# Optimization experiments

Hardware: AMD Instinct MI355X
Metric: run time of the kernel (lower is better)

## Reference

```python
import jax, jax.numpy as jnp
import numpy as np

DELTA = 0.1


def setup_inputs() -> dict:
    key = jax.random.key(0)
    k1, k2 = jax.random.split(key)
    B, T_text, adim, T_feats = 16, 512, 256, 4096
    hs = jax.random.normal(k1, (B, T_text, adim), dtype=jnp.float32)
    ds = jax.random.uniform(k2, (B, T_text), dtype=jnp.float32) * 8.0  # durations in frames
    h_masks = jnp.ones((B, T_feats), dtype=bool)
    d_masks = jnp.ones((B, T_text), dtype=bool)
    return {"hs": hs, "ds": ds, "h_masks": h_masks, "d_masks": d_masks}


def reference(hs, ds, h_masks, d_masks):
    # hs: (B, T_text, adim), ds: (B, T_text), h_masks: (B, T_feats), d_masks: (B, T_text)
    B, T_feats = h_masks.shape
    t = jnp.arange(T_feats, dtype=jnp.float32)[None, :] * h_masks.astype(jnp.float32)  # (B, T_feats)
    c = jnp.cumsum(ds, axis=-1) - ds / 2  # token centers (B, T_text)
    # energy: (B, T_feats, T_text) -- the large broadcast intermediate
    energy = -DELTA * (t[:, :, None] - c[:, None, :]) ** 2
    energy = jnp.where(d_masks[:, None, :], energy, -jnp.inf)
    p_attn = jax.nn.softmax(energy, axis=2)  # (B, T_feats, T_text)
    return jnp.einsum('bft,bta->bfa', p_attn, hs)  # (B, T_feats, adim)
```

## Files before the change

### kernel.cpp

```cpp
#include <hip/hip_runtime.h>


namespace {
constexpr int kB = 16;
constexpr int kT = 512;
constexpr int kA = 256;
constexpr int kF = 4096;
constexpr float kDelta = 0.1f;
constexpr int kFTile = 16;
constexpr int kRadius = 10;
constexpr int kPad = 4;
constexpr int kMaxK = 128;
constexpr int kWStride = kFTile + 4;
typedef float f32x4 __attribute__((ext_vector_type(4)));
}

__global__ __launch_bounds__(256, 7) void upsample_kernel(
    const float* __restrict__ hs, const float* __restrict__ ds,
    const int* __restrict__ h_masks, const int* __restrict__ d_masks,
    float* __restrict__ out) {
  __shared__ __align__(16) float s_c[kT];
  __shared__ int s_dm[kT];
  __shared__ __align__(16) float s_w[kMaxK * kWStride];
  __shared__ float s_t[kFTile];
  __shared__ float s_rsum[kFTile];
  __shared__ float s_wsum[4];

  const int id = blockIdx.x;
  const int b = id & 15;
  const int f0 = (id >> 4) * kFTile;
  const int tid = threadIdx.x;
  const int wave = tid >> 6, lane = tid & 63;

  const float2 dsv = *reinterpret_cast<const float2*>(ds + (size_t)b * kT + 2 * tid);
  const float psum = dsv.x + dsv.y;
  float incl = psum;
#pragma unroll
  for (int off = 1; off < 64; off <<= 1) {
    float u = __shfl_up(incl, off, 64);
    if (lane >= off) incl += u;
  }
  if (lane == 63) s_wsum[wave] = incl;

  for (int j = tid; j < kT; j += 256) s_dm[j] = d_masks[(size_t)b * kT + j];

  const int g = tid >> 4;
  const int l = tid & 15;
  const int f = f0 + g;
  const float tf = h_masks[(size_t)b * kF + f] ? (float)f : 0.0f;
  __syncthreads();

  float basesum = 0.0f;
#pragma unroll
  for (int w = 0; w < 4; ++w)
    if (w < wave) basesum += s_wsum[w];
  const float excl = basesum + incl - psum;
  s_c[2 * tid]     = excl + 0.5f * dsv.x;
  s_c[2 * tid + 1] = excl + dsv.x + 0.5f * dsv.y;
  if (l == 0) s_t[g] = tf;
  __syncthreads();

  float tmin = s_t[0], tmax = s_t[0];
#pragma unroll
  for (int i = 1; i < kFTile; ++i) {
    tmin = fminf(tmin, s_t[i]);
    tmax = fmaxf(tmax, s_t[i]);
  }
  const float lo = tmin - (float)kRadius;
  const float hi = tmax + (float)kRadius;
  int alo = 0, elo = kT;
  int ahi = 0, ehi = kT;
#pragma unroll
  for (int it = 0; it < 9; ++it) {
    const int m1 = (alo + elo) >> 1;
    const int m2 = (ahi + ehi) >> 1;
    const float c1 = s_c[m1];
    const float c2 = s_c[m2];
    if (alo < elo) { if (c1 < lo) alo = m1 + 1; else elo = m1; }
    if (ahi < ehi) { if (c2 <= hi) ahi = m2 + 1; else ehi = m2; }
  }
  int jlo = max(0, alo - kPad);
  int jhi = min(kT, ahi + kPad);
  int K = jhi - jlo;
  if (K > kMaxK) {
    jlo += (K - kMaxK) >> 1;
    jhi = jlo + kMaxK;
    K = kMaxK;
  }
  {
    const int ext = (4 - (K & 3)) & 3;
    if (jhi + ext <= kT) jhi += ext; else jlo -= ext;
    K += ext;
  }

  float m = -1e38f;
  for (int jj = l; jj < K; jj += 16) {
    const int j = jlo + jj;
    const float d = tf - s_c[j];
    float e = -kDelta * d * d;
    if (!s_dm[j]) e = -1e30f;
    s_w[jj * kWStride + g] = e;
    m = fmaxf(m, e);
  }
#pragma unroll
  for (int off = 8; off >= 1; off >>= 1) m = fmaxf(m, __shfl_xor(m, off, 16));
  float ssum = 0.0f;
  for (int jj = l; jj < K; jj += 16) {
    const float w = __expf(s_w[jj * kWStride + g] - m);
    s_w[jj * kWStride + g] = w;
    ssum += w;
  }
#pragma unroll
  for (int off = 8; off >= 1; off >>= 1) ssum += __shfl_xor(ssum, off, 16);
  if (l == 0) s_rsum[g] = 1.0f / ssum;
  __syncthreads();

  const int q = tid >> 6;
  const int ch = (tid & 63) << 2;
  const float* hp = hs + ((size_t)b * kT + jlo) * kA + ch;
  const float* wp = s_w + 4 * q;
  float acc[4][4];
#pragma unroll
  for (int i = 0; i < 4; ++i)
#pragma unroll
    for (int k = 0; k < 4; ++k) acc[i][k] = 0.0f;

  for (int jj = 0; jj < K; jj += 4) {
    const float4 h0 = *reinterpret_cast<const float4*>(hp);
    const float4 h1 = *reinterpret_cast<const float4*>(hp + kA);
    const float4 h2 = *reinterpret_cast<const float4*>(hp + 2 * kA);
    const float4 h3 = *reinterpret_cast<const float4*>(hp + 3 * kA);
    const float4 w0 = *reinterpret_cast<const float4*>(wp);
    const float4 w1 = *reinterpret_cast<const float4*>(wp + kWStride);
    const float4 w2 = *reinterpret_cast<const float4*>(wp + 2 * kWStride);
    const float4 w3 = *reinterpret_cast<const float4*>(wp + 3 * kWStride);
    const float hf0[4] = {h0.x, h0.y, h0.z, h0.w};
    const float hf1[4] = {h1.x, h1.y, h1.z, h1.w};
    const float hf2[4] = {h2.x, h2.y, h2.z, h2.w};
    const float hf3[4] = {h3.x, h3.y, h3.z, h3.w};
    const float wf0[4] = {w0.x, w0.y, w0.z, w0.w};
    const float wf1[4] = {w1.x, w1.y, w1.z, w1.w};
    const float wf2[4] = {w2.x, w2.y, w2.z, w2.w};
    const float wf3[4] = {w3.x, w3.y, w3.z, w3.w};
#pragma unroll
    for (int i = 0; i < 4; ++i)
#pragma unroll
      for (int k = 0; k < 4; ++k) {
        acc[i][k] += wf0[i] * hf0[k];
        acc[i][k] += wf1[i] * hf1[k];
        acc[i][k] += wf2[i] * hf2[k];
        acc[i][k] += wf3[i] * hf3[k];
      }
    hp += 4 * kA;
    wp += 4 * kWStride;
  }

  float* ob = out + ((size_t)b * kF + (size_t)(f0 + 4 * q)) * kA + ch;
#pragma unroll
  for (int i = 0; i < 4; ++i) {
    const float r = s_rsum[4 * q + i];
    f32x4 o;
    o.x = acc[i][0] * r; o.y = acc[i][1] * r;
    o.z = acc[i][2] * r; o.w = acc[i][3] * r;
    __builtin_nontemporal_store(o, reinterpret_cast<f32x4*>(ob + (size_t)i * kA));
  }
}

extern "C" void kernel_launch(void* const* d_in, const int* in_sizes, int n_in,
                              void* d_out, int out_size, void* d_ws, size_t ws_size,
                              hipStream_t stream) {
  const float* hs = (const float*)d_in[0];
  const float* ds = (const float*)d_in[1];
  const int* h_masks = (const int*)d_in[2];
  const int* d_masks = (const int*)d_in[3];
  float* out = (float*)d_out;

  upsample_kernel<<<kB * (kF / kFTile), 256, 0, stream>>>(hs, ds, h_masks, d_masks, out);
}
```

Measured before the change: 92.10 us.

## Double frame tile to 32 per block and prefetch hs rows in GEMV loop

Each block now handles 32 output frames instead of 16, so every thread accumulates 8 frames by 4 channels and each loaded hs row is reused across twice as many frames. The softmax phase is regrouped to 8 lanes per frame, and the hs loads for the next 4 tokens are issued before the current FMAs to hide global latency. In exchange the per-block token window K grows, as it must span 32 frames, and the larger accumulator raises register pressure, so occupancy is lowered from 7 to 5 blocks per CU. The window is still capped at 128 tokens, and the kPad and kRadius margins are unchanged.

```diff
diff --git a/kernel.cpp b/kernel.cpp
--- a/kernel.cpp
+++ b/kernel.cpp
@@ -7,7 +7,7 @@
 constexpr int kA = 256;
 constexpr int kF = 4096;
 constexpr float kDelta = 0.1f;
-constexpr int kFTile = 16;
+constexpr int kFTile = 32;
 constexpr int kRadius = 10;
 constexpr int kPad = 4;
 constexpr int kMaxK = 128;
@@ -15,7 +15,7 @@
 typedef float f32x4 __attribute__((ext_vector_type(4)));
 }
 
-__global__ __launch_bounds__(256, 7) void upsample_kernel(
+__global__ __launch_bounds__(256, 5) void upsample_kernel(
     const float* __restrict__ hs, const float* __restrict__ ds,
     const int* __restrict__ h_masks, const int* __restrict__ d_masks,
     float* __restrict__ out) {
@@ -43,11 +43,10 @@
   if (lane == 63) s_wsum[wave] = incl;
 
   for (int j = tid; j < kT; j += 256) s_dm[j] = d_masks[(size_t)b * kT + j];
-
-  const int g = tid >> 4;
-  const int l = tid & 15;
-  const int f = f0 + g;
-  const float tf = h_masks[(size_t)b * kF + f] ? (float)f : 0.0f;
+  if (tid < kFTile) {
+    const int f = f0 + tid;
+    s_t[tid] = h_masks[(size_t)b * kF + f] ? (float)f : 0.0f;
+  }
   __syncthreads();
 
   float basesum = 0.0f;
@@ -57,7 +56,6 @@
   const float excl = basesum + incl - psum;
   s_c[2 * tid]     = excl + 0.5f * dsv.x;
   s_c[2 * tid + 1] = excl + dsv.x + 0.5f * dsv.y;
-  if (l == 0) s_t[g] = tf;
   __syncthreads();
 
   float tmin = s_t[0], tmax = s_t[0];
@@ -93,8 +91,11 @@
     K += ext;
   }
 
+  const int g = tid >> 3;
+  const int l = tid & 7;
+  const float tf = s_t[g];
   float m = -1e38f;
-  for (int jj = l; jj < K; jj += 16) {
+  for (int jj = l; jj < K; jj += 8) {
     const int j = jlo + jj;
     const float d = tf - s_c[j];
     float e = -kDelta * d * d;
@@ -103,62 +104,60 @@
     m = fmaxf(m, e);
   }
 #pragma unroll
-  for (int off = 8; off >= 1; off >>= 1) m = fmaxf(m, __shfl_xor(m, off, 16));
+  for (int off = 4; off >= 1; off >>= 1) m = fmaxf(m, __shfl_xor(m, off, 8));
   float ssum = 0.0f;
-  for (int jj = l; jj < K; jj += 16) {
+  for (int jj = l; jj < K; jj += 8) {
     const float w = __expf(s_w[jj * kWStride + g] - m);
     s_w[jj * kWStride + g] = w;
     ssum += w;
   }
 #pragma unroll
-  for (int off = 8; off >= 1; off >>= 1) ssum += __shfl_xor(ssum, off, 16);
+  for (int off = 4; off >= 1; off >>= 1) ssum += __shfl_xor(ssum, off, 8);
   if (l == 0) s_rsum[g] = 1.0f / ssum;
   __syncthreads();
 
   const int q = tid >> 6;
   const int ch = (tid & 63) << 2;
   const float* hp = hs + ((size_t)b * kT + jlo) * kA + ch;
-  const float* wp = s_w + 4 * q;
-  float acc[4][4];
+  float acc[8][4];
 #pragma unroll
-  for (int i = 0; i < 4; ++i)
+  for (int i = 0; i < 8; ++i)
 #pragma unroll
     for (int k = 0; k < 4; ++k) acc[i][k] = 0.0f;
 
+  f32x4 h0 = *reinterpret_cast<const f32x4*>(hp);
+  f32x4 h1 = *reinterpret_cast<const f32x4*>(hp + kA);
+  f32x4 h2 = *reinterpret_cast<const f32x4*>(hp + 2 * kA);
+  f32x4 h3 = *reinterpret_cast<const f32x4*>(hp + 3 * kA);
+
   for (int jj = 0; jj < K; jj += 4) {
-    const float4 h0 = *reinterpret_cast<const float4*>(hp);
-    const float4 h1 = *reinterpret_cast<const float4*>(hp + kA);
-    const float4 h2 = *reinterpret_cast<const float4*>(hp + 2 * kA);
-    const float4 h3 = *reinterpret_cast<const float4*>(hp + 3 * kA);
-    const float4 w0 = *reinterpret_cast<const float4*>(wp);
-    const float4 w1 = *reinterpret_cast<const float4*>(wp + kWStride);
-    const float4 w2 = *reinterpret_cast<const float4*>(wp + 2 * kWStride);
-    const float4 w3 = *reinterpret_cast<const float4*>(wp + 3 * kWStride);
-    const float hf0[4] = {h0.x, h0.y, h0.z, h0.w};
-    const float hf1[4] = {h1.x, h1.y, h1.z, h1.w};
-    const float hf2[4] = {h2.x, h2.y, h2.z, h2.w};
-    const float hf3[4] = {h3.x, h3.y, h3.z, h3.w};
-    const float wf0[4] = {w0.x, w0.y, w0.z, w0.w};
-    const float wf1[4] = {w1.x, w1.y, w1.z, w1.w};
-    const float wf2[4] = {w2.x, w2.y, w2.z, w2.w};
-    const float wf3[4] = {w3.x, w3.y, w3.z, w3.w};
+    const float* hpn = hp + ((jj + 4 < K) ? 4 * kA : 0);
+    const f32x4 n0 = *reinterpret_cast<const f32x4*>(hpn);
+    const f32x4 n1 = *reinterpret_cast<const f32x4*>(hpn + kA);
+    const f32x4 n2 = *reinterpret_cast<const f32x4*>(hpn + 2 * kA);
+    const f32x4 n3 = *reinterpret_cast<const f32x4*>(hpn + 3 * kA);
+
+    const float* wb = s_w + jj * kWStride + 8 * q;
 #pragma unroll
-    for (int i = 0; i < 4; ++i)
+    for (int mm = 0; mm < 4; ++mm) {
+      const f32x4 wlo = *reinterpret_cast<const f32x4*>(wb + mm * kWStride);
+      const f32x4 whi = *reinterpret_cast<const f32x4*>(wb + mm * kWStride + 4);
+      const f32x4 hm = (mm == 0) ? h0 : (mm == 1) ? h1 : (mm == 2) ? h2 : h3;
+      const float hf[4] = {hm.x, hm.y, hm.z, hm.w};
+      const float wf[8] = {wlo.x, wlo.y, wlo.z, wlo.w, whi.x, whi.y, whi.z, whi.w};
 #pragma unroll
-      for (int k = 0; k < 4; ++k) {
-        acc[i][k] += wf0[i] * hf0[k];
-        acc[i][k] += wf1[i] * hf1[k];
-        acc[i][k] += wf2[i] * hf2[k];
-        acc[i][k] += wf3[i] * hf3[k];
-      }
-    hp += 4 * kA;
-    wp += 4 * kWStride;
+      for (int i = 0; i < 8; ++i)
+#pragma unroll
+        for (int k = 0; k < 4; ++k) acc[i][k] += wf[i] * hf[k];
+    }
+    h0 = n0; h1 = n1; h2 = n2; h3 = n3;
+    hp = hpn;
   }
 
-  float* ob = out + ((size_t)b * kF + (size_t)(f0 + 4 * q)) * kA + ch;
+  float* ob = out + ((size_t)b * kF + (size_t)(f0 + 8 * q)) * kA + ch;
 #pragma unroll
-  for (int i = 0; i < 4; ++i) {
-    const float r = s_rsum[4 * q + i];
+  for (int i = 0; i < 8; ++i) {
+    const float r = s_rsum[8 * q + i];
     f32x4 o;
     o.x = acc[i][0] * r; o.y = acc[i][1] * r;
     o.z = acc[i][2] * r; o.w = acc[i][3] * r;
```

New measurement: 92.48 us. Within noise of the previous version (+0.4%).
